# Kernel tuning notes

Measured on AMD Instinct MI355X. Metric: run time of the kernel, lower is better.

## Reference

```python
import jax, jax.numpy as jnp
import numpy as np

N_NODES = 50000
N_EDGES = 800000
NFEAT = 128
NHID = 128
NCLASS = 2


def _glorot(key, shape):
    fan_in, fan_out = shape[0], shape[1]
    lim = np.sqrt(6.0 / (fan_in + fan_out)).astype(np.float32)
    return jax.random.uniform(key, shape, jnp.float32, -lim, lim)


def setup_inputs() -> dict:
    key = jax.random.key(0)
    ks = jax.random.split(key, 12)
    x = jax.random.normal(ks[0], (N_NODES, NFEAT), jnp.float32)
    edge_src = jax.random.randint(ks[1], (N_EDGES,), 0, N_NODES, jnp.int64)
    edge_dst = jax.random.randint(ks[2], (N_EDGES,), 0, N_NODES, jnp.int64)
    return {
        "x": x,
        "edge_src": edge_src,
        "edge_dst": edge_dst,
        "W1_self": _glorot(ks[3], (NFEAT, NHID)),
        "W1_neigh": _glorot(ks[4], (NFEAT, NHID)),
        "b1": jnp.zeros((NHID,), jnp.float32),
        "W2_self": _glorot(ks[5], (NHID, NHID)),
        "W2_neigh": _glorot(ks[6], (NHID, NHID)),
        "b2": jnp.zeros((NHID,), jnp.float32),
        "Wf": _glorot(ks[7], (NHID, NCLASS)),
        "bf": jnp.zeros((NCLASS,), jnp.float32),
    }


def _mean_neigh(h, edge_src, edge_dst):
    # gather source features per edge, segment-mean into destination nodes
    msgs = h[edge_src]                                   # [E, d]
    summed = jax.ops.segment_sum(msgs, edge_dst, num_segments=N_NODES)  # [N, d]
    deg = jax.ops.segment_sum(jnp.ones((edge_dst.shape[0],), h.dtype), edge_dst,
                              num_segments=N_NODES)      # [N]
    return summed / jnp.maximum(deg, 1.0)[:, None]


def _sage_conv(h, edge_src, edge_dst, W_self, W_neigh, b):
    h_neigh = _mean_neigh(h, edge_src, edge_dst)
    return h @ W_self + h_neigh @ W_neigh + b


def reference(x, edge_src, edge_dst, W1_self, W1_neigh, b1,
              W2_self, W2_neigh, b2, Wf, bf):
    h = jax.nn.relu(_sage_conv(x, edge_src, edge_dst, W1_self, W1_neigh, b1))
    # dropout is identity in eval mode
    h = _sage_conv(h, edge_src, edge_dst, W2_self, W2_neigh, b2)
    return h @ Wf + bf
```

## Files before the change

kernel.cpp:

```cpp
#include <hip/hip_runtime.h>
#include <cstdint>
#include <cstddef>

#define N_NODES 50000
#define N_EDGES 800000
#define CAP 64

#define BIN_SZ 512
#define NBIN 98
#define NSLOT 64

#define CHUNK_A 2048
#define N_PARTS 391

#define NB_PART N_PARTS
#define NB_PACK 128
#define NB_COMB 2
#define NB_PRE  (NB_PART + NB_PACK + NB_COMB)

#define NB_GEMM 391
#define NB_MAIN (NBIN * 5)

#define NB_AGG 13312

typedef __attribute__((ext_vector_type(8))) short bf16x8;
typedef __attribute__((ext_vector_type(4))) float f32x4;
typedef __attribute__((ext_vector_type(2))) float f32x2;
typedef __attribute__((ext_vector_type(4))) int   i32x4;

__device__ __forceinline__ unsigned short f2bf(float f) {
    unsigned u = __builtin_bit_cast(unsigned, f);
    u += 0x7fff + ((u >> 16) & 1);
    return (unsigned short)(u >> 16);
}
__device__ __forceinline__ float bflo(unsigned u) { return __builtin_bit_cast(float, u << 16); }
__device__ __forceinline__ float bfhi(unsigned u) { return __builtin_bit_cast(float, u & 0xffff0000u); }

__device__ __forceinline__ unsigned char f2fp8_sw(float f) {
    unsigned u = __builtin_bit_cast(unsigned, f);
    unsigned s = (u >> 24) & 0x80;
    unsigned a = u & 0x7fffffffu;
    if (a < 0x3c800000u) return (unsigned char)s;
    if (a > 0x43e00000u) a = 0x43e00000u;
    unsigned lsb = (a >> 20) & 1;
    a += 0x7ffffu + lsb;
    unsigned e = (a >> 23) - 120;
    unsigned m = (a >> 20) & 7;
    return (unsigned char)(s | (e << 3) | m);
}
__device__ __forceinline__ float fp82f_sw(unsigned b) {
    unsigned s = (b & 0x80u) << 24;
    unsigned e = (b >> 3) & 15, m = b & 7;
    if (e == 0) {
        float v = (float)m * 0.001953125f;
        return (b & 0x80u) ? -v : v;
    }
    return __builtin_bit_cast(float, s | ((e + 120) << 23) | (m << 20));
}
__device__ __forceinline__ unsigned short pk_fp8(float a, float b) {
#if __has_builtin(__builtin_amdgcn_cvt_pk_fp8_f32)
    return (unsigned short)__builtin_amdgcn_cvt_pk_fp8_f32(a, b, 0u, false);
#else
    return (unsigned short)(f2fp8_sw(a) | ((unsigned)f2fp8_sw(b) << 8));
#endif
}
__device__ __forceinline__ f32x2 unpk_fp8(unsigned short v) {
#if __has_builtin(__builtin_amdgcn_cvt_pk_f32_fp8)
    return __builtin_amdgcn_cvt_pk_f32_fp8((unsigned)v, false);
#else
    f32x2 r; r[0] = fp82f_sw(v & 0xffu); r[1] = fp82f_sw(v >> 8); return r;
#endif
}

__global__ __launch_bounds__(256) void k_pre(const int* __restrict__ src,
                                             const int* __restrict__ dst,
                                             const float* __restrict__ W1s,
                                             const float* __restrict__ W1n,
                                             const float* __restrict__ W2s,
                                             const float* __restrict__ W2n,
                                             const float* __restrict__ b2,
                                             const float* __restrict__ Wf,
                                             const float* __restrict__ bf,
                                             unsigned* __restrict__ seg,
                                             int* __restrict__ segcnt,
                                             unsigned short* __restrict__ wpack,
                                             float* __restrict__ wc) {
    int blk = blockIdx.x;
    int tid = threadIdx.x;

    if (blk < NB_PART) {
        __shared__ int hist[NBIN];
        for (int i = tid; i < NBIN; i += 256) hist[i] = 0;
        __syncthreads();
        int g = blk;
        int e0 = g * CHUNK_A + tid * 8;
        bool v = e0 < N_EDGES;
        i32x4 da = {0,0,0,0}, db = da, sa = da, sb = da;
        if (v) {
            da = *(const i32x4*)(dst + e0);
            db = *(const i32x4*)(dst + e0 + 4);
            sa = *(const i32x4*)(src + e0);
            sb = *(const i32x4*)(src + e0 + 4);
        }
        int d[8], s[8];
#pragma unroll
        for (int j = 0; j < 4; ++j) { d[j] = da[j]; s[j] = sa[j]; d[4 + j] = db[j]; s[4 + j] = sb[j]; }
#pragma unroll
        for (int j = 0; j < 8; ++j) {
            if (v) {
                int b = (int)((unsigned)d[j] >> 9);
                int lpos = atomicAdd(&hist[b], 1);
                if (lpos < NSLOT)
                    seg[((size_t)b * N_PARTS + g) * NSLOT + lpos] =
                        ((unsigned)d[j] << 16) | (unsigned)s[j];
            }
        }
        __syncthreads();
        for (int i = tid; i < NBIN; i += 256) {
            int h = hist[i];
            segcnt[i * N_PARTS + g] = h < NSLOT ? h : NSLOT;
        }
    } else if (blk < NB_PART + NB_PACK) {
        int idx = (blk - NB_PART) * 256 + tid;
        int j = idx & 7;
        int lane = (idx >> 3) & 63;
        int ks = (idx >> 9) & 7;
        int nt = idx >> 12;
        int krow = ks * 32 + ((lane >> 4) << 3) + j;
        int col = nt * 16 + (lane & 15);
        float v = (krow < 128) ? W1s[krow * 128 + col] : W1n[(krow - 128) * 128 + col];
        wpack[idx] = f2bf(v);
    } else {
        int role = blk - NB_PART - NB_PACK;
        int k = tid >> 1, c = tid & 1;
        const float* W = role == 0 ? W2s : W2n;
        float s = 0.f;
        for (int j = 0; j < 128; ++j) s += W[k * 128 + j] * Wf[j * 2 + c];
        wc[role * 256 + k * 2 + c] = s;
        if (role == 1 && tid < 2) {
            float sb = bf[tid];
            for (int j = 0; j < 128; ++j) sb += b2[j] * Wf[j * 2 + tid];
            wc[512 + tid] = sb;
        }
    }
}

__global__ __launch_bounds__(512) void k_main(const float* __restrict__ x,
                                              const unsigned* __restrict__ seg,
                                              const int* __restrict__ segcnt,
                                              const unsigned short* __restrict__ wpack,
                                              const float* __restrict__ b1,
                                              int* __restrict__ cnt,
                                              unsigned short* __restrict__ bucket,
                                              unsigned short* __restrict__ zb,
                                              unsigned char* __restrict__ yb8) {
    int blk = blockIdx.x;
    int tid = threadIdx.x;
    int G = blk / 5;
    int pos = blk - G * 5;

    if (pos == 0) {
        int b = G;
        __shared__ int cur[BIN_SZ];
        __shared__ int scnt[N_PARTS];
        for (int i = tid; i < BIN_SZ; i += 512) cur[i] = 0;
        for (int i = tid; i < N_PARTS; i += 512) scnt[i] = segcnt[b * N_PARTS + i];
        __syncthreads();
        int wave = tid >> 6, lane = tid & 63;
        const unsigned* segb = seg + (size_t)b * N_PARTS * NSLOT;
        for (int j = 0; j < 13; ++j) {
            unsigned v[4];
#pragma unroll
            for (int t = 0; t < 4; ++t) {
                int p = wave + 8 * (j * 4 + t);
                int n = p < N_PARTS ? scnt[p] : 0;
                v[t] = lane < n ? segb[(size_t)p * NSLOT + lane] : 0xffffffffu;
            }
#pragma unroll
            for (int t = 0; t < 4; ++t) {
                if (v[t] != 0xffffffffu) {
                    int d = (int)(v[t] >> 16);
                    int p = atomicAdd(&cur[d & (BIN_SZ - 1)], 1);
                    if (p < CAP) bucket[(size_t)d * CAP + p] = (unsigned short)(v[t] & 0xffffu);
                }
            }
        }
        __syncthreads();
        for (int i = tid; i < BIN_SZ; i += 512) {
            int node = (b << 9) + i;
            if (node < N_NODES) cnt[node] = cur[i];
        }
    } else {
        int g4 = G * 4 + (pos - 1);
        if (g4 >= NB_GEMM) return;
        int wid = tid >> 6;
        int lane = tid & 63;
        int l15 = lane & 15;
        int rowBase = g4 * 128 + wid * 16;
        int arow = rowBase + l15;
        if (arow >= N_NODES) arow = N_NODES - 1;
        int koff = (lane >> 4) << 3;

        const float* xrow = x + (size_t)arow * 128 + koff;
        bf16x8 a[4];
#pragma unroll
        for (int ks = 0; ks < 4; ++ks) {
            f32x4 f0 = *(const f32x4*)(xrow + ks * 32);
            f32x4 f1 = *(const f32x4*)(xrow + ks * 32 + 4);
            bf16x8 t;
            t[0] = (short)f2bf(f0[0]); t[1] = (short)f2bf(f0[1]);
            t[2] = (short)f2bf(f0[2]); t[3] = (short)f2bf(f0[3]);
            t[4] = (short)f2bf(f1[0]); t[5] = (short)f2bf(f1[1]);
            t[6] = (short)f2bf(f1[2]); t[7] = (short)f2bf(f1[3]);
            a[ks] = t;
        }

        f32x4 zacc[8] = {};
        f32x4 yacc[8] = {};
        const bf16x8* wp = (const bf16x8*)wpack + lane;
        __builtin_amdgcn_s_setprio(1);
#pragma unroll
        for (int nt = 0; nt < 8; ++nt) {
#pragma unroll
            for (int ks = 0; ks < 4; ++ks)
                zacc[nt] = __builtin_amdgcn_mfma_f32_16x16x32_bf16(a[ks], wp[(nt * 8 + ks) * 64], zacc[nt], 0, 0, 0);
#pragma unroll
            for (int ks = 0; ks < 4; ++ks)
                yacc[nt] = __builtin_amdgcn_mfma_f32_16x16x32_bf16(a[ks], wp[(nt * 8 + 4 + ks) * 64], yacc[nt], 0, 0, 0);
        }
        __builtin_amdgcn_s_setprio(0);

        int crow0 = rowBase + ((lane >> 4) << 2);
#pragma unroll
        for (int k = 0; k < 4; ++k) {
            int colA = k * 32 + l15;
            float biasA = b1[colA];
            float biasB = b1[colA + 16];
            int p2 = k * 16 + l15;
#pragma unroll
            for (int r = 0; r < 4; ++r) {
                int row = crow0 + r;
                if (row < N_NODES) {
                    unsigned zu = (unsigned)f2bf(zacc[2 * k][r] + biasA) |
                                  ((unsigned)f2bf(zacc[2 * k + 1][r] + biasB) << 16);
                    *(unsigned*)(zb + (size_t)row * 128 + 2 * p2) = zu;
                    *(unsigned short*)(yb8 + (size_t)row * 128 + 2 * p2) =
                        pk_fp8(yacc[2 * k][r], yacc[2 * k + 1][r]);
                }
            }
        }
    }
}

__global__ __launch_bounds__(256) void k_agg2(const unsigned char* __restrict__ yb8,
                                              const unsigned short* __restrict__ zb,
                                              const int* __restrict__ cnt,
                                              const unsigned short* __restrict__ bucket,
                                              const float* __restrict__ wc,
                                              float* __restrict__ pq) {
    int blk = blockIdx.x;
    int wavein = threadIdx.x >> 6;
    int lane = threadIdx.x & 63;
    int xcd = blk & 7;
    int i = (blk >> 3) * 4 + wavein;
    int b = xcd + ((i >> 9) << 3);
    if (b >= NBIN) return;
    int node = (b << 9) + (i & 511);
    if (node >= N_NODES) return;

    int deg = cnt[node];
    int colA = ((lane >> 4) << 5) + (lane & 15);
    int colB = colA + 16;
    unsigned zu = *(const unsigned*)(zb + (size_t)node * 128 + 2 * lane);
    float2 wsA = *(const float2*)(wc + 2 * colA);
    float2 wsB = *(const float2*)(wc + 2 * colB);
    float2 wnA = *(const float2*)(wc + 256 + 2 * colA);
    float2 wnB = *(const float2*)(wc + 256 + 2 * colB);

    int n = deg < CAP ? deg : CAP;
    const unsigned short* bk = bucket + (size_t)node * CAP;
    const unsigned char* ybl = yb8 + 2 * lane;
    float ax0 = 0.f, ay0 = 0.f, ax1 = 0.f, ay1 = 0.f;
    float ax2 = 0.f, ay2 = 0.f, ax3 = 0.f, ay3 = 0.f;
    int e = 0;
    for (; e + 16 <= n; e += 16) {
        uint4 ia = *(const uint4*)(bk + e);
        uint4 ib = *(const uint4*)(bk + e + 8);
        int s0  = ia.x & 0xffff, s1  = ia.x >> 16, s2  = ia.y & 0xffff, s3  = ia.y >> 16;
        int s4  = ia.z & 0xffff, s5  = ia.z >> 16, s6  = ia.w & 0xffff, s7  = ia.w >> 16;
        int s8  = ib.x & 0xffff, s9  = ib.x >> 16, s10 = ib.y & 0xffff, s11 = ib.y >> 16;
        int s12 = ib.z & 0xffff, s13 = ib.z >> 16, s14 = ib.w & 0xffff, s15 = ib.w >> 16;
        unsigned short t0  = *(const unsigned short*)(ybl + (size_t)s0  * 128);
        unsigned short t1  = *(const unsigned short*)(ybl + (size_t)s1  * 128);
        unsigned short t2  = *(const unsigned short*)(ybl + (size_t)s2  * 128);
        unsigned short t3  = *(const unsigned short*)(ybl + (size_t)s3  * 128);
        unsigned short t4  = *(const unsigned short*)(ybl + (size_t)s4  * 128);
        unsigned short t5  = *(const unsigned short*)(ybl + (size_t)s5  * 128);
        unsigned short t6  = *(const unsigned short*)(ybl + (size_t)s6  * 128);
        unsigned short t7  = *(const unsigned short*)(ybl + (size_t)s7  * 128);
        unsigned short t8  = *(const unsigned short*)(ybl + (size_t)s8  * 128);
        unsigned short t9  = *(const unsigned short*)(ybl + (size_t)s9  * 128);
        unsigned short t10 = *(const unsigned short*)(ybl + (size_t)s10 * 128);
        unsigned short t11 = *(const unsigned short*)(ybl + (size_t)s11 * 128);
        unsigned short t12 = *(const unsigned short*)(ybl + (size_t)s12 * 128);
        unsigned short t13 = *(const unsigned short*)(ybl + (size_t)s13 * 128);
        unsigned short t14 = *(const unsigned short*)(ybl + (size_t)s14 * 128);
        unsigned short t15 = *(const unsigned short*)(ybl + (size_t)s15 * 128);
        f32x2 v0 = unpk_fp8(t0),  v1 = unpk_fp8(t1),  v2 = unpk_fp8(t2),  v3 = unpk_fp8(t3);
        f32x2 v4 = unpk_fp8(t4),  v5 = unpk_fp8(t5),  v6 = unpk_fp8(t6),  v7 = unpk_fp8(t7);
        f32x2 v8 = unpk_fp8(t8),  v9 = unpk_fp8(t9),  v10 = unpk_fp8(t10), v11 = unpk_fp8(t11);
        f32x2 v12 = unpk_fp8(t12), v13 = unpk_fp8(t13), v14 = unpk_fp8(t14), v15 = unpk_fp8(t15);
        ax0 += v0[0];  ay0 += v0[1];  ax1 += v1[0];  ay1 += v1[1];
        ax2 += v2[0];  ay2 += v2[1];  ax3 += v3[0];  ay3 += v3[1];
        ax0 += v4[0];  ay0 += v4[1];  ax1 += v5[0];  ay1 += v5[1];
        ax2 += v6[0];  ay2 += v6[1];  ax3 += v7[0];  ay3 += v7[1];
        ax0 += v8[0];  ay0 += v8[1];  ax1 += v9[0];  ay1 += v9[1];
        ax2 += v10[0]; ay2 += v10[1]; ax3 += v11[0]; ay3 += v11[1];
        ax0 += v12[0]; ay0 += v12[1]; ax1 += v13[0]; ay1 += v13[1];
        ax2 += v14[0]; ay2 += v14[1]; ax3 += v15[0]; ay3 += v15[1];
    }
    if (e + 8 <= n) {
        uint4 ia = *(const uint4*)(bk + e);
        int s0 = ia.x & 0xffff, s1 = ia.x >> 16, s2 = ia.y & 0xffff, s3 = ia.y >> 16;
        int s4 = ia.z & 0xffff, s5 = ia.z >> 16, s6 = ia.w & 0xffff, s7 = ia.w >> 16;
        unsigned short t0 = *(const unsigned short*)(ybl + (size_t)s0 * 128);
        unsigned short t1 = *(const unsigned short*)(ybl + (size_t)s1 * 128);
        unsigned short t2 = *(const unsigned short*)(ybl + (size_t)s2 * 128);
        unsigned short t3 = *(const unsigned short*)(ybl + (size_t)s3 * 128);
        unsigned short t4 = *(const unsigned short*)(ybl + (size_t)s4 * 128);
        unsigned short t5 = *(const unsigned short*)(ybl + (size_t)s5 * 128);
        unsigned short t6 = *(const unsigned short*)(ybl + (size_t)s6 * 128);
        unsigned short t7 = *(const unsigned short*)(ybl + (size_t)s7 * 128);
        f32x2 v0 = unpk_fp8(t0), v1 = unpk_fp8(t1), v2 = unpk_fp8(t2), v3 = unpk_fp8(t3);
        f32x2 v4 = unpk_fp8(t4), v5 = unpk_fp8(t5), v6 = unpk_fp8(t6), v7 = unpk_fp8(t7);
        ax0 += v0[0]; ay0 += v0[1]; ax1 += v1[0]; ay1 += v1[1];
        ax2 += v2[0]; ay2 += v2[1]; ax3 += v3[0]; ay3 += v3[1];
        ax0 += v4[0]; ay0 += v4[1]; ax1 += v5[0]; ay1 += v5[1];
        ax2 += v6[0]; ay2 += v6[1]; ax3 += v7[0]; ay3 += v7[1];
        e += 8;
    }
    if (e + 4 <= n) {
        uint2 ia = *(const uint2*)(bk + e);
        int s0 = ia.x & 0xffff, s1 = ia.x >> 16, s2 = ia.y & 0xffff, s3 = ia.y >> 16;
        unsigned short t0 = *(const unsigned short*)(ybl + (size_t)s0 * 128);
        unsigned short t1 = *(const unsigned short*)(ybl + (size_t)s1 * 128);
        unsigned short t2 = *(const unsigned short*)(ybl + (size_t)s2 * 128);
        unsigned short t3 = *(const unsigned short*)(ybl + (size_t)s3 * 128);
        f32x2 v0 = unpk_fp8(t0), v1 = unpk_fp8(t1), v2 = unpk_fp8(t2), v3 = unpk_fp8(t3);
        ax0 += v0[0]; ay0 += v0[1]; ax1 += v1[0]; ay1 += v1[1];
        ax2 += v2[0]; ay2 += v2[1]; ax3 += v3[0]; ay3 += v3[1];
        e += 4;
    }
    for (; e < n; ++e) {
        unsigned short t = *(const unsigned short*)(ybl + (size_t)bk[e] * 128);
        f32x2 v = unpk_fp8(t);
        ax0 += v[0]; ay0 += v[1];
    }
    float inv = 1.0f / fmaxf((float)deg, 1.0f);
    float mx = ((ax0 + ax1) + (ax2 + ax3)) * inv;
    float my = ((ay0 + ay1) + (ay2 + ay3)) * inv;

    float h0 = fmaxf(bflo(zu) + mx, 0.f);
    float h1v = fmaxf(bfhi(zu) + my, 0.f);

    float p0 = h0 * wsA.x + h1v * wsB.x;
    float p1 = h0 * wsA.y + h1v * wsB.y;
    float q0 = h0 * wnA.x + h1v * wnB.x;
    float q1 = h0 * wnA.y + h1v * wnB.y;
#pragma unroll
    for (int off = 32; off >= 1; off >>= 1) {
        p0 += __shfl_xor(p0, off, 64);
        p1 += __shfl_xor(p1, off, 64);
        q0 += __shfl_xor(q0, off, 64);
        q1 += __shfl_xor(q1, off, 64);
    }
    if (lane == 0) {
        float4 o; o.x = p0; o.y = p1; o.z = q0; o.w = q1;
        ((float4*)pq)[node] = o;
    }
}

__global__ __launch_bounds__(256) void k_final(const float* __restrict__ pq,
                                               const int* __restrict__ cnt,
                                               const unsigned short* __restrict__ bucket,
                                               const float* __restrict__ wc,
                                               float* __restrict__ out) {
    int blk = blockIdx.x;
    int wavein = threadIdx.x >> 6;
    int lane = threadIdx.x & 63;
    int xcd = blk & 7;
    int i = (blk >> 3) * 4 + wavein;
    int b = xcd + ((i >> 9) << 3);
    if (b >= NBIN) return;
    int node = (b << 9) + (i & 511);
    if (node >= N_NODES) return;

    int deg = cnt[node];
    int n = deg < CAP ? deg : CAP;
    float qx = 0.f, qy = 0.f;
    if (lane < n) {
        int s = bucket[(size_t)node * CAP + lane];
        float2 q = *(const float2*)(pq + (size_t)s * 4 + 2);
        qx = q.x; qy = q.y;
    }
#pragma unroll
    for (int off = 32; off >= 1; off >>= 1) {
        qx += __shfl_xor(qx, off, 64);
        qy += __shfl_xor(qy, off, 64);
    }
    if (lane == 0) {
        float inv = 1.0f / fmaxf((float)deg, 1.0f);
        float2 p = *(const float2*)(pq + (size_t)node * 4);
        out[(size_t)node * 2 + 0] = p.x + qx * inv + wc[512];
        out[(size_t)node * 2 + 1] = p.y + qy * inv + wc[513];
    }
}

extern "C" void kernel_launch(void* const* d_in, const int* in_sizes, int n_in,
                              void* d_out, int out_size, void* d_ws, size_t ws_size,
                              hipStream_t stream) {
    const float* x   = (const float*)d_in[0];
    const int* esrc  = (const int*)d_in[1];
    const int* edst  = (const int*)d_in[2];
    const float* W1s = (const float*)d_in[3];
    const float* W1n = (const float*)d_in[4];
    const float* b1  = (const float*)d_in[5];
    const float* W2s = (const float*)d_in[6];
    const float* W2n = (const float*)d_in[7];
    const float* b2  = (const float*)d_in[8];
    const float* Wf  = (const float*)d_in[9];
    const float* bf  = (const float*)d_in[10];
    float* out = (float*)d_out;

    char* ws = (char*)d_ws;
    auto alloc = [&](size_t bytes) {
        char* p = ws;
        ws += (bytes + 255) & ~(size_t)255;
        return p;
    };
    int*            cnt    = (int*)           alloc((size_t)N_NODES * 4);
    unsigned short* bucket = (unsigned short*)alloc((size_t)N_NODES * CAP * 2);
    unsigned*       seg    = (unsigned*)      alloc((size_t)NBIN * N_PARTS * NSLOT * 4);
    int*            segcnt = (int*)           alloc((size_t)NBIN * N_PARTS * 4);
    unsigned short* zb     = (unsigned short*)alloc((size_t)N_NODES * 128 * 2);
    unsigned char*  yb8    = (unsigned char*) alloc((size_t)N_NODES * 128);
    unsigned short* wpack  = (unsigned short*)alloc(8 * 8 * 64 * 8 * 2);
    float*          pq     = (float*)         alloc((size_t)N_NODES * 4 * 4);
    float*          wc     = (float*)         alloc(1024 * 4);

    k_pre<<<NB_PRE, 256, 0, stream>>>(esrc, edst, W1s, W1n, W2s, W2n, b2, Wf, bf,
                                      seg, segcnt, wpack, wc);
    k_main<<<NB_MAIN, 512, 0, stream>>>(x, seg, segcnt, wpack, b1, cnt, bucket, zb, yb8);
    k_agg2<<<NB_AGG, 256, 0, stream>>>(yb8, zb, cnt, bucket, wc, pq);
    k_final<<<NB_AGG, 256, 0, stream>>>(pq, cnt, bucket, wc, out);
}
```

Before: 77.56 us.

## Merge four kernel launches into one persistent cooperative kernel with grid syncs

Replaces the four separate launches (partition/pack, bucket+GEMM, layer-2 aggregation, final aggregation) with a single cooperative persistent kernel that loops over tasks and uses grid.sync between phases. The goal is to remove launch overhead and inter-kernel gaps. In exchange the grid size is capped by occupancy, so each block iterates over many tasks. Grid-wide barriers and lower parallelism in the gather phases could cost more than the launch savings.

```diff
diff --git a/kernel.cpp b/kernel.cpp
--- a/kernel.cpp
+++ b/kernel.cpp
@@ -1,6 +1,9 @@
 #include <hip/hip_runtime.h>
+#include <hip/hip_cooperative_groups.h>
 #include <cstdint>
 #include <cstddef>
+
+namespace cg = cooperative_groups;
 
 #define N_NODES 50000
 #define N_EDGES 800000
@@ -13,15 +16,12 @@
 #define CHUNK_A 2048
 #define N_PARTS 391
 
-#define NB_PART N_PARTS
-#define NB_PACK 128
+#define NB_PACK 64
 #define NB_COMB 2
-#define NB_PRE  (NB_PART + NB_PACK + NB_COMB)
+#define NTASK_A (N_PARTS + NB_PACK + NB_COMB)
 
 #define NB_GEMM 391
-#define NB_MAIN (NBIN * 5)
-
-#define NB_AGG 13312
+#define NTASK_B (NBIN + NB_GEMM)
 
 typedef __attribute__((ext_vector_type(8))) short bf16x8;
 typedef __attribute__((ext_vector_type(4))) float f32x4;
@@ -72,347 +72,335 @@
 #endif
 }
 
-__global__ __launch_bounds__(256) void k_pre(const int* __restrict__ src,
+__global__ __launch_bounds__(512) void k_all(const float* __restrict__ x,
+                                             const int* __restrict__ src,
                                              const int* __restrict__ dst,
                                              const float* __restrict__ W1s,
                                              const float* __restrict__ W1n,
+                                             const float* __restrict__ b1,
                                              const float* __restrict__ W2s,
                                              const float* __restrict__ W2n,
                                              const float* __restrict__ b2,
                                              const float* __restrict__ Wf,
                                              const float* __restrict__ bf,
+                                             int* __restrict__ cnt,
+                                             unsigned short* __restrict__ bucket,
                                              unsigned* __restrict__ seg,
                                              int* __restrict__ segcnt,
+                                             unsigned short* __restrict__ zb,
+                                             unsigned char* __restrict__ yb8,
                                              unsigned short* __restrict__ wpack,
-                                             float* __restrict__ wc) {
+                                             float* __restrict__ wc,
+                                             float* __restrict__ pq,
+                                             float* __restrict__ out) {
+    cg::grid_group grid = cg::this_grid();
+    __shared__ int smem[1024];
     int blk = blockIdx.x;
+    int G = gridDim.x;
     int tid = threadIdx.x;
-
-    if (blk < NB_PART) {
-        __shared__ int hist[NBIN];
-        for (int i = tid; i < NBIN; i += 256) hist[i] = 0;
-        __syncthreads();
-        int g = blk;
-        int e0 = g * CHUNK_A + tid * 8;
-        bool v = e0 < N_EDGES;
-        i32x4 da = {0,0,0,0}, db = da, sa = da, sb = da;
-        if (v) {
-            da = *(const i32x4*)(dst + e0);
-            db = *(const i32x4*)(dst + e0 + 4);
-            sa = *(const i32x4*)(src + e0);
-            sb = *(const i32x4*)(src + e0 + 4);
-        }
-        int d[8], s[8];
-#pragma unroll
-        for (int j = 0; j < 4; ++j) { d[j] = da[j]; s[j] = sa[j]; d[4 + j] = db[j]; s[4 + j] = sb[j]; }
-#pragma unroll
-        for (int j = 0; j < 8; ++j) {
+    int wavein = tid >> 6;
+    int lane = tid & 63;
+
+    for (int task = blk; task < NTASK_A; task += G) {
+        if (task < N_PARTS) {
+            __syncthreads();
+            for (int i = tid; i < NBIN; i += 512) smem[i] = 0;
+            __syncthreads();
+            int e0 = task * CHUNK_A + tid * 4;
+            bool v = e0 < N_EDGES;
+            i32x4 d4 = {0,0,0,0}, s4 = d4;
             if (v) {
-                int b = (int)((unsigned)d[j] >> 9);
-                int lpos = atomicAdd(&hist[b], 1);
-                if (lpos < NSLOT)
-                    seg[((size_t)b * N_PARTS + g) * NSLOT + lpos] =
-                        ((unsigned)d[j] << 16) | (unsigned)s[j];
-            }
-        }
-        __syncthreads();
-        for (int i = tid; i < NBIN; i += 256) {
-            int h = hist[i];
-            segcnt[i * N_PARTS + g] = h < NSLOT ? h : NSLOT;
-        }
-    } else if (blk < NB_PART + NB_PACK) {
-        int idx = (blk - NB_PART) * 256 + tid;
-        int j = idx & 7;
-        int lane = (idx >> 3) & 63;
-        int ks = (idx >> 9) & 7;
-        int nt = idx >> 12;
-        int krow = ks * 32 + ((lane >> 4) << 3) + j;
-        int col = nt * 16 + (lane & 15);
-        float v = (krow < 128) ? W1s[krow * 128 + col] : W1n[(krow - 128) * 128 + col];
-        wpack[idx] = f2bf(v);
-    } else {
-        int role = blk - NB_PART - NB_PACK;
-        int k = tid >> 1, c = tid & 1;
-        const float* W = role == 0 ? W2s : W2n;
-        float s = 0.f;
-        for (int j = 0; j < 128; ++j) s += W[k * 128 + j] * Wf[j * 2 + c];
-        wc[role * 256 + k * 2 + c] = s;
-        if (role == 1 && tid < 2) {
-            float sb = bf[tid];
-            for (int j = 0; j < 128; ++j) sb += b2[j] * Wf[j * 2 + tid];
-            wc[512 + tid] = sb;
+                d4 = *(const i32x4*)(dst + e0);
+                s4 = *(const i32x4*)(src + e0);
+            }
+#pragma unroll
+            for (int j = 0; j < 4; ++j) {
+                if (v) {
+                    int b = (int)((unsigned)d4[j] >> 9);
+                    int lpos = atomicAdd(&smem[b], 1);
+                    if (lpos < NSLOT)
+                        seg[((size_t)b * N_PARTS + task) * NSLOT + lpos] =
+                            ((unsigned)d4[j] << 16) | (unsigned)s4[j];
+                }
+            }
+            __syncthreads();
+            for (int i = tid; i < NBIN; i += 512) {
+                int h = smem[i];
+                segcnt[i * N_PARTS + task] = h < NSLOT ? h : NSLOT;
+            }
+        } else if (task < N_PARTS + NB_PACK) {
+            int idx = (task - N_PARTS) * 512 + tid;
+            int j = idx & 7;
+            int ln = (idx >> 3) & 63;
+            int ks = (idx >> 9) & 7;
+            int nt = idx >> 12;
+            int krow = ks * 32 + ((ln >> 4) << 3) + j;
+            int col = nt * 16 + (ln & 15);
+            float v = (krow < 128) ? W1s[krow * 128 + col] : W1n[(krow - 128) * 128 + col];
+            wpack[idx] = f2bf(v);
+        } else {
+            int role = task - N_PARTS - NB_PACK;
+            if (tid < 256) {
+                int k = tid >> 1, c = tid & 1;
+                const float* W = role == 0 ? W2s : W2n;
+                float s = 0.f;
+                for (int j = 0; j < 128; ++j) s += W[k * 128 + j] * Wf[j * 2 + c];
+                wc[role * 256 + k * 2 + c] = s;
+                if (role == 1 && tid < 2) {
+                    float sb = bf[tid];
+                    for (int j = 0; j < 128; ++j) sb += b2[j] * Wf[j * 2 + tid];
+                    wc[512 + tid] = sb;
+                }
+            }
         }
     }
-}
-
-__global__ __launch_bounds__(512) void k_main(const float* __restrict__ x,
-                                              const unsigned* __restrict__ seg,
-                                              const int* __restrict__ segcnt,
-                                              const unsigned short* __restrict__ wpack,
-                                              const float* __restrict__ b1,
-                                              int* __restrict__ cnt,
-                                              unsigned short* __restrict__ bucket,
-                                              unsigned short* __restrict__ zb,
-                                              unsigned char* __restrict__ yb8) {
-    int blk = blockIdx.x;
-    int tid = threadIdx.x;
-    int G = blk / 5;
-    int pos = blk - G * 5;
-
-    if (pos == 0) {
-        int b = G;
-        __shared__ int cur[BIN_SZ];
-        __shared__ int scnt[N_PARTS];
-        for (int i = tid; i < BIN_SZ; i += 512) cur[i] = 0;
-        for (int i = tid; i < N_PARTS; i += 512) scnt[i] = segcnt[b * N_PARTS + i];
-        __syncthreads();
-        int wave = tid >> 6, lane = tid & 63;
-        const unsigned* segb = seg + (size_t)b * N_PARTS * NSLOT;
-        for (int j = 0; j < 13; ++j) {
-            unsigned v[4];
-#pragma unroll
-            for (int t = 0; t < 4; ++t) {
-                int p = wave + 8 * (j * 4 + t);
-                int n = p < N_PARTS ? scnt[p] : 0;
-                v[t] = lane < n ? segb[(size_t)p * NSLOT + lane] : 0xffffffffu;
-            }
-#pragma unroll
-            for (int t = 0; t < 4; ++t) {
-                if (v[t] != 0xffffffffu) {
-                    int d = (int)(v[t] >> 16);
-                    int p = atomicAdd(&cur[d & (BIN_SZ - 1)], 1);
-                    if (p < CAP) bucket[(size_t)d * CAP + p] = (unsigned short)(v[t] & 0xffffu);
+    grid.sync();
+
+    for (int task = blk; task < NTASK_B; task += G) {
+        if (task < NBIN) {
+            int b = task;
+            int* cur = smem;
+            int* scnt = smem + BIN_SZ;
+            __syncthreads();
+            for (int i = tid; i < BIN_SZ; i += 512) cur[i] = 0;
+            for (int i = tid; i < N_PARTS; i += 512) scnt[i] = segcnt[b * N_PARTS + i];
+            __syncthreads();
+            const unsigned* segb = seg + (size_t)b * N_PARTS * NSLOT;
+            for (int j = 0; j < 13; ++j) {
+                unsigned v[4];
+#pragma unroll
+                for (int t = 0; t < 4; ++t) {
+                    int p = wavein + 8 * (j * 4 + t);
+                    int n = p < N_PARTS ? scnt[p] : 0;
+                    v[t] = lane < n ? segb[(size_t)p * NSLOT + lane] : 0xffffffffu;
                 }
-            }
-        }
-        __syncthreads();
-        for (int i = tid; i < BIN_SZ; i += 512) {
-            int node = (b << 9) + i;
-            if (node < N_NODES) cnt[node] = cur[i];
-        }
-    } else {
-        int g4 = G * 4 + (pos - 1);
-        if (g4 >= NB_GEMM) return;
-        int wid = tid >> 6;
-        int lane = tid & 63;
-        int l15 = lane & 15;
-        int rowBase = g4 * 128 + wid * 16;
-        int arow = rowBase + l15;
-        if (arow >= N_NODES) arow = N_NODES - 1;
-        int koff = (lane >> 4) << 3;
-
-        const float* xrow = x + (size_t)arow * 128 + koff;
-        bf16x8 a[4];
-#pragma unroll
-        for (int ks = 0; ks < 4; ++ks) {
-            f32x4 f0 = *(const f32x4*)(xrow + ks * 32);
-            f32x4 f1 = *(const f32x4*)(xrow + ks * 32 + 4);
-            bf16x8 t;
-            t[0] = (short)f2bf(f0[0]); t[1] = (short)f2bf(f0[1]);
-            t[2] = (short)f2bf(f0[2]); t[3] = (short)f2bf(f0[3]);
-            t[4] = (short)f2bf(f1[0]); t[5] = (short)f2bf(f1[1]);
-            t[6] = (short)f2bf(f1[2]); t[7] = (short)f2bf(f1[3]);
-            a[ks] = t;
-        }
-
-        f32x4 zacc[8] = {};
-        f32x4 yacc[8] = {};
-        const bf16x8* wp = (const bf16x8*)wpack + lane;
-        __builtin_amdgcn_s_setprio(1);
-#pragma unroll
-        for (int nt = 0; nt < 8; ++nt) {
-#pragma unroll
-            for (int ks = 0; ks < 4; ++ks)
-                zacc[nt] = __builtin_amdgcn_mfma_f32_16x16x32_bf16(a[ks], wp[(nt * 8 + ks) * 64], zacc[nt], 0, 0, 0);
-#pragma unroll
-            for (int ks = 0; ks < 4; ++ks)
-                yacc[nt] = __builtin_amdgcn_mfma_f32_16x16x32_bf16(a[ks], wp[(nt * 8 + 4 + ks) * 64], yacc[nt], 0, 0, 0);
-        }
-        __builtin_amdgcn_s_setprio(0);
-
-        int crow0 = rowBase + ((lane >> 4) << 2);
-#pragma unroll
-        for (int k = 0; k < 4; ++k) {
-            int colA = k * 32 + l15;
-            float biasA = b1[colA];
-            float biasB = b1[colA + 16];
-            int p2 = k * 16 + l15;
-#pragma unroll
-            for (int r = 0; r < 4; ++r) {
-                int row = crow0 + r;
-                if (row < N_NODES) {
-                    unsigned zu = (unsigned)f2bf(zacc[2 * k][r] + biasA) |
-                                  ((unsigned)f2bf(zacc[2 * k + 1][r] + biasB) << 16);
-                    *(unsigned*)(zb + (size_t)row * 128 + 2 * p2) = zu;
-                    *(unsigned short*)(yb8 + (size_t)row * 128 + 2 * p2) =
-                        pk_fp8(yacc[2 * k][r], yacc[2 * k + 1][r]);
+#pragma unroll
+                for (int t = 0; t < 4; ++t) {
+                    if (v[t] != 0xffffffffu) {
+                        int d = (int)(v[t] >> 16);
+                        int p = atomicAdd(&cur[d & (BIN_SZ - 1)], 1);
+                        if (p < CAP) bucket[(size_t)d * CAP + p] = (unsigned short)(v[t] & 0xffffu);
+                    }
+                }
+            }
+            __syncthreads();
+            for (int i = tid; i < BIN_SZ; i += 512) {
+                int node = (b << 9) + i;
+                if (node < N_NODES) cnt[node] = cur[i];
+            }
+        } else {
+            int g4 = task - NBIN;
+            int l15 = lane & 15;
+            int rowBase = g4 * 128 + wavein * 16;
+            int arow = rowBase + l15;
+            if (arow >= N_NODES) arow = N_NODES - 1;
+            int koff = (lane >> 4) << 3;
+
+            const float* xrow = x + (size_t)arow * 128 + koff;
+            bf16x8 a[4];
+#pragma unroll
+            for (int ks = 0; ks < 4; ++ks) {
+                f32x4 f0 = *(const f32x4*)(xrow + ks * 32);
+                f32x4 f1 = *(const f32x4*)(xrow + ks * 32 + 4);
+                bf16x8 t;
+                t[0] = (short)f2bf(f0[0]); t[1] = (short)f2bf(f0[1]);
+                t[2] = (short)f2bf(f0[2]); t[3] = (short)f2bf(f0[3]);
+                t[4] = (short)f2bf(f1[0]); t[5] = (short)f2bf(f1[1]);
+                t[6] = (short)f2bf(f1[2]); t[7] = (short)f2bf(f1[3]);
+                a[ks] = t;
+            }
+
+            f32x4 zacc[8] = {};
+            f32x4 yacc[8] = {};
+            const bf16x8* wp = (const bf16x8*)wpack + lane;
+            __builtin_amdgcn_s_setprio(1);
+#pragma unroll
+            for (int nt = 0; nt < 8; ++nt) {
+#pragma unroll
+                for (int ks = 0; ks < 4; ++ks)
+                    zacc[nt] = __builtin_amdgcn_mfma_f32_16x16x32_bf16(a[ks], wp[(nt * 8 + ks) * 64], zacc[nt], 0, 0, 0);
+#pragma unroll
+                for (int ks = 0; ks < 4; ++ks)
+                    yacc[nt] = __builtin_amdgcn_mfma_f32_16x16x32_bf16(a[ks], wp[(nt * 8 + 4 + ks) * 64], yacc[nt], 0, 0, 0);
+            }
+            __builtin_amdgcn_s_setprio(0);
+
+            int crow0 = rowBase + ((lane >> 4) << 2);
+#pragma unroll
+            for (int k = 0; k < 4; ++k) {
+                int colA = k * 32 + l15;
+                float biasA = b1[colA];
+                float biasB = b1[colA + 16];
+                int p2 = k * 16 + l15;
+#pragma unroll
+                for (int r = 0; r < 4; ++r) {
+                    int row = crow0 + r;
+                    if (row < N_NODES) {
+                        unsigned zu = (unsigned)f2bf(zacc[2 * k][r] + biasA) |
+                                      ((unsigned)f2bf(zacc[2 * k + 1][r] + biasB) << 16);
+                        *(unsigned*)(zb + (size_t)row * 128 + 2 * p2) = zu;
+                        *(unsigned short*)(yb8 + (size_t)row * 128 + 2 * p2) =
+                            pk_fp8(yacc[2 * k][r], yacc[2 * k + 1][r]);
+                    }
                 }
             }
         }
     }
-}
-
-__global__ __launch_bounds__(256) void k_agg2(const unsigned char* __restrict__ yb8,
-                                              const unsigned short* __restrict__ zb,
-                                              const int* __restrict__ cnt,
-                                              const unsigned short* __restrict__ bucket,
-                                              const float* __restrict__ wc,
-                                              float* __restrict__ pq) {
-    int blk = blockIdx.x;
-    int wavein = threadIdx.x >> 6;
-    int lane = threadIdx.x & 63;
-    int xcd = blk & 7;
-    int i = (blk >> 3) * 4 + wavein;
-    int b = xcd + ((i >> 9) << 3);
-    if (b >= NBIN) return;
-    int node = (b << 9) + (i & 511);
-    if (node >= N_NODES) return;
-
-    int deg = cnt[node];
-    int colA = ((lane >> 4) << 5) + (lane & 15);
-    int colB = colA + 16;
-    unsigned zu = *(const unsigned*)(zb + (size_t)node * 128 + 2 * lane);
-    float2 wsA = *(const float2*)(wc + 2 * colA);
-    float2 wsB = *(const float2*)(wc + 2 * colB);
-    float2 wnA = *(const float2*)(wc + 256 + 2 * colA);
-    float2 wnB = *(const float2*)(wc + 256 + 2 * colB);
-
-    int n = deg < CAP ? deg : CAP;
-    const unsigned short* bk = bucket + (size_t)node * CAP;
-    const unsigned char* ybl = yb8 + 2 * lane;
-    float ax0 = 0.f, ay0 = 0.f, ax1 = 0.f, ay1 = 0.f;
-    float ax2 = 0.f, ay2 = 0.f, ax3 = 0.f, ay3 = 0.f;
-    int e = 0;
-    for (; e + 16 <= n; e += 16) {
-        uint4 ia = *(const uint4*)(bk + e);
-        uint4 ib = *(const uint4*)(bk + e + 8);
-        int s0  = ia.x & 0xffff, s1  = ia.x >> 16, s2  = ia.y & 0xffff, s3  = ia.y >> 16;
-        int s4  = ia.z & 0xffff, s5  = ia.z >> 16, s6  = ia.w & 0xffff, s7  = ia.w >> 16;
-        int s8  = ib.x & 0xffff, s9  = ib.x >> 16, s10 = ib.y & 0xffff, s11 = ib.y >> 16;
-        int s12 = ib.z & 0xffff, s13 = ib.z >> 16, s14 = ib.w & 0xffff, s15 = ib.w >> 16;
-        unsigned short t0  = *(const unsigned short*)(ybl + (size_t)s0  * 128);
-        unsigned short t1  = *(const unsigned short*)(ybl + (size_t)s1  * 128);
-        unsigned short t2  = *(const unsigned short*)(ybl + (size_t)s2  * 128);
-        unsigned short t3  = *(const unsigned short*)(ybl + (size_t)s3  * 128);
-        unsigned short t4  = *(const unsigned short*)(ybl + (size_t)s4  * 128);
-        unsigned short t5  = *(const unsigned short*)(ybl + (size_t)s5  * 128);
-        unsigned short t6  = *(const unsigned short*)(ybl + (size_t)s6  * 128);
-        unsigned short t7  = *(const unsigned short*)(ybl + (size_t)s7  * 128);
-        unsigned short t8  = *(const unsigned short*)(ybl + (size_t)s8  * 128);
-        unsigned short t9  = *(const unsigned short*)(ybl + (size_t)s9  * 128);
-        unsigned short t10 = *(const unsigned short*)(ybl + (size_t)s10 * 128);
-        unsigned short t11 = *(const unsigned short*)(ybl + (size_t)s11 * 128);
-        unsigned short t12 = *(const unsigned short*)(ybl + (size_t)s12 * 128);
-        unsigned short t13 = *(const unsigned short*)(ybl + (size_t)s13 * 128);
-        unsigned short t14 = *(const unsigned short*)(ybl + (size_t)s14 * 128);
-        unsigned short t15 = *(const unsigned short*)(ybl + (size_t)s15 * 128);
-        f32x2 v0 = unpk_fp8(t0),  v1 = unpk_fp8(t1),  v2 = unpk_fp8(t2),  v3 = unpk_fp8(t3);
-        f32x2 v4 = unpk_fp8(t4),  v5 = unpk_fp8(t5),  v6 = unpk_fp8(t6),  v7 = unpk_fp8(t7);
-        f32x2 v8 = unpk_fp8(t8),  v9 = unpk_fp8(t9),  v10 = unpk_fp8(t10), v11 = unpk_fp8(t11);
-        f32x2 v12 = unpk_fp8(t12), v13 = unpk_fp8(t13), v14 = unpk_fp8(t14), v15 = unpk_fp8(t15);
-        ax0 += v0[0];  ay0 += v0[1];  ax1 += v1[0];  ay1 += v1[1];
-        ax2 += v2[0];  ay2 += v2[1];  ax3 += v3[0];  ay3 += v3[1];
-        ax0 += v4[0];  ay0 += v4[1];  ax1 += v5[0];  ay1 += v5[1];
-        ax2 += v6[0];  ay2 += v6[1];  ax3 += v7[0];  ay3 += v7[1];
-        ax0 += v8[0];  ay0 += v8[1];  ax1 += v9[0];  ay1 += v9[1];
-        ax2 += v10[0]; ay2 += v10[1]; ax3 += v11[0]; ay3 += v11[1];
-        ax0 += v12[0]; ay0 += v12[1]; ax1 += v13[0]; ay1 += v13[1];
-        ax2 += v14[0]; ay2 += v14[1]; ax3 += v15[0]; ay3 += v15[1];
+    grid.sync();
+
+    {
+        int xcd = blk & 7;
+        int wstride = (G >> 3) * 8;
+        for (int i = (blk >> 3) * 8 + wavein; i < 13 * 512; i += wstride) {
+            int b = xcd + ((i >> 9) << 3);
+            if (b >= NBIN) break;
+            int node = (b << 9) + (i & 511);
+            if (node >= N_NODES) continue;
+
+            int deg = cnt[node];
+            int colA = ((lane >> 4) << 5) + (lane & 15);
+            int colB = colA + 16;
+            unsigned zu = *(const unsigned*)(zb + (size_t)node * 128 + 2 * lane);
+            float2 wsA = *(const float2*)(wc + 2 * colA);
+            float2 wsB = *(const float2*)(wc + 2 * colB);
+            float2 wnA = *(const float2*)(wc + 256 + 2 * colA);
+            float2 wnB = *(const float2*)(wc + 256 + 2 * colB);
+
+            int n = deg < CAP ? deg : CAP;
+            const unsigned short* bk = bucket + (size_t)node * CAP;
+            const unsigned char* ybl = yb8 + 2 * lane;
+            float ax0 = 0.f, ay0 = 0.f, ax1 = 0.f, ay1 = 0.f;
+            float ax2 = 0.f, ay2 = 0.f, ax3 = 0.f, ay3 = 0.f;
+            int e = 0;
+            for (; e + 16 <= n; e += 16) {
+                uint4 ia = *(const uint4*)(bk + e);
+                uint4 ib = *(const uint4*)(bk + e + 8);
+                int s0  = ia.x & 0xffff, s1  = ia.x >> 16, s2  = ia.y & 0xffff, s3  = ia.y >> 16;
+                int s4  = ia.z & 0xffff, s5  = ia.z >> 16, s6  = ia.w & 0xffff, s7  = ia.w >> 16;
+                int s8  = ib.x & 0xffff, s9  = ib.x >> 16, s10 = ib.y & 0xffff, s11 = ib.y >> 16;
+                int s12 = ib.z & 0xffff, s13 = ib.z >> 16, s14 = ib.w & 0xffff, s15 = ib.w >> 16;
+                unsigned short t0  = *(const unsigned short*)(ybl + (size_t)s0  * 128);
+                unsigned short t1  = *(const unsigned short*)(ybl + (size_t)s1  * 128);
+                unsigned short t2  = *(const unsigned short*)(ybl + (size_t)s2  * 128);
+                unsigned short t3  = *(const unsigned short*)(ybl + (size_t)s3  * 128);
+                unsigned short t4  = *(const unsigned short*)(ybl + (size_t)s4  * 128);
+                unsigned short t5  = *(const unsigned short*)(ybl + (size_t)s5  * 128);
+                unsigned short t6  = *(const unsigned short*)(ybl + (size_t)s6  * 128);
+                unsigned short t7  = *(const unsigned short*)(ybl + (size_t)s7  * 128);
+                unsigned short t8  = *(const unsigned short*)(ybl + (size_t)s8  * 128);
+                unsigned short t9  = *(const unsigned short*)(ybl + (size_t)s9  * 128);
+                unsigned short t10 = *(const unsigned short*)(ybl + (size_t)s10 * 128);
+                unsigned short t11 = *(const unsigned short*)(ybl + (size_t)s11 * 128);
+                unsigned short t12 = *(const unsigned short*)(ybl + (size_t)s12 * 128);
+                unsigned short t13 = *(const unsigned short*)(ybl + (size_t)s13 * 128);
+                unsigned short t14 = *(const unsigned short*)(ybl + (size_t)s14 * 128);
+                unsigned short t15 = *(const unsigned short*)(ybl + (size_t)s15 * 128);
+                f32x2 v0 = unpk_fp8(t0),  v1 = unpk_fp8(t1),  v2 = unpk_fp8(t2),  v3 = unpk_fp8(t3);
+                f32x2 v4 = unpk_fp8(t4),  v5 = unpk_fp8(t5),  v6 = unpk_fp8(t6),  v7 = unpk_fp8(t7);
+                f32x2 v8 = unpk_fp8(t8),  v9 = unpk_fp8(t9),  v10 = unpk_fp8(t10), v11 = unpk_fp8(t11);
+                f32x2 v12 = unpk_fp8(t12), v13 = unpk_fp8(t13), v14 = unpk_fp8(t14), v15 = unpk_fp8(t15);
+                ax0 += v0[0];  ay0 += v0[1];  ax1 += v1[0];  ay1 += v1[1];
+                ax2 += v2[0];  ay2 += v2[1];  ax3 += v3[0];  ay3 += v3[1];
+                ax0 += v4[0];  ay0 += v4[1];  ax1 += v5[0];  ay1 += v5[1];
+                ax2 += v6[0];  ay2 += v6[1];  ax3 += v7[0];  ay3 += v7[1];
+                ax0 += v8[0];  ay0 += v8[1];  ax1 += v9[0];  ay1 += v9[1];
+                ax2 += v10[0]; ay2 += v10[1]; ax3 += v11[0]; ay3 += v11[1];
+                ax0 += v12[0]; ay0 += v12[1]; ax1 += v13[0]; ay1 += v13[1];
+                ax2 += v14[0]; ay2 += v14[1]; ax3 += v15[0]; ay3 += v15[1];
+            }
+            if (e + 8 <= n) {
+                uint4 ia = *(const uint4*)(bk + e);
+                int s0 = ia.x & 0xffff, s1 = ia.x >> 16, s2 = ia.y & 0xffff, s3 = ia.y >> 16;
+                int s4 = ia.z & 0xffff, s5 = ia.z >> 16, s6 = ia.w & 0xffff, s7 = ia.w >> 16;
+                unsigned short t0 = *(const unsigned short*)(ybl + (size_t)s0 * 128);
+                unsigned short t1 = *(const unsigned short*)(ybl + (size_t)s1 * 128);
+                unsigned short t2 = *(const unsigned short*)(ybl + (size_t)s2 * 128);
+                unsigned short t3 = *(const unsigned short*)(ybl + (size_t)s3 * 128);
+                unsigned short t4 = *(const unsigned short*)(ybl + (size_t)s4 * 128);
+                unsigned short t5 = *(const unsigned short*)(ybl + (size_t)s5 * 128);
+                unsigned short t6 = *(const unsigned short*)(ybl + (size_t)s6 * 128);
+                unsigned short t7 = *(const unsigned short*)(ybl + (size_t)s7 * 128);
+                f32x2 v0 = unpk_fp8(t0), v1 = unpk_fp8(t1), v2 = unpk_fp8(t2), v3 = unpk_fp8(t3);
+                f32x2 v4 = unpk_fp8(t4), v5 = unpk_fp8(t5), v6 = unpk_fp8(t6), v7 = unpk_fp8(t7);
+                ax0 += v0[0]; ay0 += v0[1]; ax1 += v1[0]; ay1 += v1[1];
+                ax2 += v2[0]; ay2 += v2[1]; ax3 += v3[0]; ay3 += v3[1];
+                ax0 += v4[0]; ay0 += v4[1]; ax1 += v5[0]; ay1 += v5[1];
+                ax2 += v6[0]; ay2 += v6[1]; ax3 += v7[0]; ay3 += v7[1];
+                e += 8;
+            }
+            if (e + 4 <= n) {
+                uint2 ia = *(const uint2*)(bk + e);
+                int s0 = ia.x & 0xffff, s1 = ia.x >> 16, s2 = ia.y & 0xffff, s3 = ia.y >> 16;
+                unsigned short t0 = *(const unsigned short*)(ybl + (size_t)s0 * 128);
+                unsigned short t1 = *(const unsigned short*)(ybl + (size_t)s1 * 128);
+                unsigned short t2 = *(const unsigned short*)(ybl + (size_t)s2 * 128);
+                unsigned short t3 = *(const unsigned short*)(ybl + (size_t)s3 * 128);
+                f32x2 v0 = unpk_fp8(t0), v1 = unpk_fp8(t1), v2 = unpk_fp8(t2), v3 = unpk_fp8(t3);
+                ax0 += v0[0]; ay0 += v0[1]; ax1 += v1[0]; ay1 += v1[1];
+                ax2 += v2[0]; ay2 += v2[1]; ax3 += v3[0]; ay3 += v3[1];
+                e += 4;
+            }
+            for (; e < n; ++e) {
+                unsigned short t = *(const unsigned short*)(ybl + (size_t)bk[e] * 128);
+                f32x2 v = unpk_fp8(t);
+                ax0 += v[0]; ay0 += v[1];
+            }
+            float inv = 1.0f / fmaxf((float)deg, 1.0f);
+            float mx = ((ax0 + ax1) + (ax2 + ax3)) * inv;
+            float my = ((ay0 + ay1) + (ay2 + ay3)) * inv;
+
+            float h0 = fmaxf(bflo(zu) + mx, 0.f);
+            float h1v = fmaxf(bfhi(zu) + my, 0.f);
+
+            float p0 = h0 * wsA.x + h1v * wsB.x;
+            float p1 = h0 * wsA.y + h1v * wsB.y;
+            float q0 = h0 * wnA.x + h1v * wnB.x;
+            float q1 = h0 * wnA.y + h1v * wnB.y;
+#pragma unroll
+            for (int off = 32; off >= 1; off >>= 1) {
+                p0 += __shfl_xor(p0, off, 64);
+                p1 += __shfl_xor(p1, off, 64);
+                q0 += __shfl_xor(q0, off, 64);
+                q1 += __shfl_xor(q1, off, 64);
+            }
+            if (lane == 0) {
+                float4 o; o.x = p0; o.y = p1; o.z = q0; o.w = q1;
+                ((float4*)pq)[node] = o;
+            }
+        }
     }
-    if (e + 8 <= n) {
-        uint4 ia = *(const uint4*)(bk + e);
-        int s0 = ia.x & 0xffff, s1 = ia.x >> 16, s2 = ia.y & 0xffff, s3 = ia.y >> 16;
-        int s4 = ia.z & 0xffff, s5 = ia.z >> 16, s6 = ia.w & 0xffff, s7 = ia.w >> 16;
-        unsigned short t0 = *(const unsigned short*)(ybl + (size_t)s0 * 128);
-        unsigned short t1 = *(const unsigned short*)(ybl + (size_t)s1 * 128);
-        unsigned short t2 = *(const unsigned short*)(ybl + (size_t)s2 * 128);
-        unsigned short t3 = *(const unsigned short*)(ybl + (size_t)s3 * 128);
-        unsigned short t4 = *(const unsigned short*)(ybl + (size_t)s4 * 128);
-        unsigned short t5 = *(const unsigned short*)(ybl + (size_t)s5 * 128);
-        unsigned short t6 = *(const unsigned short*)(ybl + (size_t)s6 * 128);
-        unsigned short t7 = *(const unsigned short*)(ybl + (size_t)s7 * 128);
-        f32x2 v0 = unpk_fp8(t0), v1 = unpk_fp8(t1), v2 = unpk_fp8(t2), v3 = unpk_fp8(t3);
-        f32x2 v4 = unpk_fp8(t4), v5 = unpk_fp8(t5), v6 = unpk_fp8(t6), v7 = unpk_fp8(t7);
-        ax0 += v0[0]; ay0 += v0[1]; ax1 += v1[0]; ay1 += v1[1];
-        ax2 += v2[0]; ay2 += v2[1]; ax3 += v3[0]; ay3 += v3[1];
-        ax0 += v4[0]; ay0 += v4[1]; ax1 += v5[0]; ay1 += v5[1];
-        ax2 += v6[0]; ay2 += v6[1]; ax3 += v7[0]; ay3 += v7[1];
-        e += 8;
-    }
-    if (e + 4 <= n) {
-        uint2 ia = *(const uint2*)(bk + e);
-        int s0 = ia.x & 0xffff, s1 = ia.x >> 16, s2 = ia.y & 0xffff, s3 = ia.y >> 16;
-        unsigned short t0 = *(const unsigned short*)(ybl + (size_t)s0 * 128);
-        unsigned short t1 = *(const unsigned short*)(ybl + (size_t)s1 * 128);
-        unsigned short t2 = *(const unsigned short*)(ybl + (size_t)s2 * 128);
-        unsigned short t3 = *(const unsigned short*)(ybl + (size_t)s3 * 128);
-        f32x2 v0 = unpk_fp8(t0), v1 = unpk_fp8(t1), v2 = unpk_fp8(t2), v3 = unpk_fp8(t3);
-        ax0 += v0[0]; ay0 += v0[1]; ax1 += v1[0]; ay1 += v1[1];
-        ax2 += v2[0]; ay2 += v2[1]; ax3 += v3[0]; ay3 += v3[1];
-        e += 4;
-    }
-    for (; e < n; ++e) {
-        unsigned short t = *(const unsigned short*)(ybl + (size_t)bk[e] * 128);
-        f32x2 v = unpk_fp8(t);
-        ax0 += v[0]; ay0 += v[1];
-    }
-    float inv = 1.0f / fmaxf((float)deg, 1.0f);
-    float mx = ((ax0 + ax1) + (ax2 + ax3)) * inv;
-    float my = ((ay0 + ay1) + (ay2 + ay3)) * inv;
-
-    float h0 = fmaxf(bflo(zu) + mx, 0.f);
-    float h1v = fmaxf(bfhi(zu) + my, 0.f);
-
-    float p0 = h0 * wsA.x + h1v * wsB.x;
-    float p1 = h0 * wsA.y + h1v * wsB.y;
-    float q0 = h0 * wnA.x + h1v * wnB.x;
-    float q1 = h0 * wnA.y + h1v * wnB.y;
-#pragma unroll
-    for (int off = 32; off >= 1; off >>= 1) {
-        p0 += __shfl_xor(p0, off, 64);
-        p1 += __shfl_xor(p1, off, 64);
-        q0 += __shfl_xor(q0, off, 64);
-        q1 += __shfl_xor(q1, off, 64);
-    }
-    if (lane == 0) {
-        float4 o; o.x = p0; o.y = p1; o.z = q0; o.w = q1;
-        ((float4*)pq)[node] = o;
-    }
-}
-
-__global__ __launch_bounds__(256) void k_final(const float* __restrict__ pq,
-                                               const int* __restrict__ cnt,
-                                               const unsigned short* __restrict__ bucket,
-                                               const float* __restrict__ wc,
-                                               float* __restrict__ out) {
-    int blk = blockIdx.x;
-    int wavein = threadIdx.x >> 6;
-    int lane = threadIdx.x & 63;
-    int xcd = blk & 7;
-    int i = (blk >> 3) * 4 + wavein;
-    int b = xcd + ((i >> 9) << 3);
-    if (b >= NBIN) return;
-    int node = (b << 9) + (i & 511);
-    if (node >= N_NODES) return;
-
-    int deg = cnt[node];
-    int n = deg < CAP ? deg : CAP;
-    float qx = 0.f, qy = 0.f;
-    if (lane < n) {
-        int s = bucket[(size_t)node * CAP + lane];
-        float2 q = *(const float2*)(pq + (size_t)s * 4 + 2);
-        qx = q.x; qy = q.y;
-    }
-#pragma unroll
-    for (int off = 32; off >= 1; off >>= 1) {
-        qx += __shfl_xor(qx, off, 64);
-        qy += __shfl_xor(qy, off, 64);
-    }
-    if (lane == 0) {
-        float inv = 1.0f / fmaxf((float)deg, 1.0f);
-        float2 p = *(const float2*)(pq + (size_t)node * 4);
-        out[(size_t)node * 2 + 0] = p.x + qx * inv + wc[512];
-        out[(size_t)node * 2 + 1] = p.y + qy * inv + wc[513];
+    grid.sync();
+
+    {
+        int xcd = blk & 7;
+        int wstride = (G >> 3) * 8;
+        float bc0 = wc[512], bc1 = wc[513];
+        for (int i = (blk >> 3) * 8 + wavein; i < 13 * 512; i += wstride) {
+            int b = xcd + ((i >> 9) << 3);
+            if (b >= NBIN) break;
+            int node = (b << 9) + (i & 511);
+            if (node >= N_NODES) continue;
+
+            int deg = cnt[node];
+            int n = deg < CAP ? deg : CAP;
+            float qx = 0.f, qy = 0.f;
+            if (lane < n) {
+                int s = bucket[(size_t)node * CAP + lane];
+                float2 q = *(const float2*)(pq + (size_t)s * 4 + 2);
+                qx = q.x; qy = q.y;
+            }
+#pragma unroll
+            for (int off = 32; off >= 1; off >>= 1) {
+                qx += __shfl_xor(qx, off, 64);
+                qy += __shfl_xor(qy, off, 64);
+            }
+            if (lane == 0) {
+                float inv = 1.0f / fmaxf((float)deg, 1.0f);
+                float2 p = *(const float2*)(pq + (size_t)node * 4);
+                out[(size_t)node * 2 + 0] = p.x + qx * inv + bc0;
+                out[(size_t)node * 2 + 1] = p.y + qy * inv + bc1;
+            }
+        }
     }
 }
 
@@ -448,9 +436,17 @@
     float*          pq     = (float*)         alloc((size_t)N_NODES * 4 * 4);
     float*          wc     = (float*)         alloc(1024 * 4);
 
-    k_pre<<<NB_PRE, 256, 0, stream>>>(esrc, edst, W1s, W1n, W2s, W2n, b2, Wf, bf,
-                                      seg, segcnt, wpack, wc);
-    k_main<<<NB_MAIN, 512, 0, stream>>>(x, seg, segcnt, wpack, b1, cnt, bucket, zb, yb8);
-    k_agg2<<<NB_AGG, 256, 0, stream>>>(yb8, zb, cnt, bucket, wc, pq);
-    k_final<<<NB_AGG, 256, 0, stream>>>(pq, cnt, bucket, wc, out);
-}
+    int nb = 0;
+    hipOccupancyMaxActiveBlocksPerMultiprocessor(&nb, (const void*)k_all, 512, 0);
+    if (nb < 1) nb = 1;
+    int G = nb * 256;
+    if (G > 1024) G = 1024;
+
+    void* kargs[] = {
+        (void*)&x, (void*)&esrc, (void*)&edst, (void*)&W1s, (void*)&W1n, (void*)&b1,
+        (void*)&W2s, (void*)&W2n, (void*)&b2, (void*)&Wf, (void*)&bf,
+        (void*)&cnt, (void*)&bucket, (void*)&seg, (void*)&segcnt,
+        (void*)&zb, (void*)&yb8, (void*)&wpack, (void*)&wc, (void*)&pq, (void*)&out
+    };
+    hipLaunchCooperativeKernel((void*)k_all, dim3(G), dim3(512), kargs, 0, stream);
+}
```

After: 253.8 us. 227% more time.
